# Optimization experiments

Hardware: AMD Instinct MI355X
Metric: run time of the kernel (lower is better)

## Reference

```python
import jax, jax.numpy as jnp
import numpy as np
from jax import lax

INPUT_SCALE = 1.0
RES_SCALE = 1.0


def setup_inputs() -> dict:
    key = jax.random.key(0)
    k1, k2, k3, k4 = jax.random.split(key, 4)
    seq_len, input_size, res_size = 4096, 512, 2048
    return {
        "input_data": jax.random.normal(k1, (seq_len, input_size), dtype=jnp.float32),
        "initial_state": jax.random.normal(k2, (res_size,), dtype=jnp.float32),
        "W_in": jax.random.normal(k3, (res_size, input_size), dtype=jnp.float32),
        "W_res": jax.random.normal(k4, (res_size, res_size), dtype=jnp.float32),
    }


def reference(input_data, initial_state, W_in, W_res):
    # state_t = tanh(input_scale * W_in @ x_t + res_scale * W_res @ state_{t-1}) / sqrt(res_size)
    res_size = W_res.shape[0]
    inv_sqrt = jnp.asarray(1.0 / np.sqrt(res_size), dtype=input_data.dtype)
    # Precompute input projection for all timesteps as one GEMM: (seq_len, res_size)
    pre = (INPUT_SCALE * input_data) @ W_in.T

    def step(state, u_t):
        new_state = jnp.tanh(u_t + RES_SCALE * (W_res @ state)) * inv_sqrt
        return new_state, new_state

    _, states = lax.scan(step, initial_state, pre)
    # (seq_len + 1, res_size): row 0 is the initial state
    return jnp.concatenate([initial_state[None, :], states], axis=0)
```

## Files before the change

### kernel.cpp

```cpp
#include <hip/hip_runtime.h>

constexpr int SEQ  = 4096;
constexpr int IN   = 512;
constexpr int RS   = 2048;
constexpr int GB   = 64;
constexpr int BT   = 1024;
constexpr int RING = 8;
constexpr float INV_SQRT = 0.022097086912079612f;

__global__ __launch_bounds__(256)
void gemm_pre_kernel(const float* __restrict__ A, const float* __restrict__ B,
                     float* __restrict__ out) {
    __shared__ float As[64][17];
    __shared__ float Bs[64][17];
    const int tid = threadIdx.x;
    const int tx = tid & 15, ty = tid >> 4;
    const int m0 = blockIdx.x * 64, n0 = blockIdx.y * 64;
    const int lr = tid >> 2;
    const int lk = (tid & 3) * 4;
    float acc[4][4] = {};
    for (int k0 = 0; k0 < IN; k0 += 16) {
        const float4 av = *(const float4*)&A[(size_t)(m0 + lr) * IN + k0 + lk];
        const float4 bv = *(const float4*)&B[(size_t)(n0 + lr) * IN + k0 + lk];
        __syncthreads();
        As[lr][lk + 0] = av.x; As[lr][lk + 1] = av.y;
        As[lr][lk + 2] = av.z; As[lr][lk + 3] = av.w;
        Bs[lr][lk + 0] = bv.x; Bs[lr][lk + 1] = bv.y;
        Bs[lr][lk + 2] = bv.z; Bs[lr][lk + 3] = bv.w;
        __syncthreads();
#pragma unroll
        for (int k = 0; k < 16; ++k) {
            float a[4], b[4];
#pragma unroll
            for (int i = 0; i < 4; ++i) a[i] = As[ty * 4 + i][k];
#pragma unroll
            for (int j = 0; j < 4; ++j) b[j] = Bs[tx * 4 + j][k];
#pragma unroll
            for (int i = 0; i < 4; ++i)
#pragma unroll
                for (int j = 0; j < 4; ++j) acc[i][j] += a[i] * b[j];
        }
    }
#pragma unroll
    for (int i = 0; i < 4; ++i) {
        float4 v = make_float4(acc[i][0], acc[i][1], acc[i][2], acc[i][3]);
        *(float4*)&out[(size_t)(m0 + ty * 4 + i + 1) * RS + n0 + tx * 4] = v;
    }
}

__device__ __forceinline__ float fast_tanh(float x) {
    float e = __expf(2.0f * x);
    return 1.0f - 2.0f * __builtin_amdgcn_rcpf(e + 1.0f);
}

#define AT_LOAD_U64(p) __hip_atomic_load((p), __ATOMIC_RELAXED, __HIP_MEMORY_SCOPE_AGENT)
#define AT_STORE_U32(p, v) __hip_atomic_store((p), (v), __ATOMIC_RELAXED, __HIP_MEMORY_SCOPE_AGENT)

__global__ __launch_bounds__(BT, 4)
void reservoir_scan_kernel(const float* __restrict__ W_res,
                           const float* __restrict__ init,
                           float* __restrict__ out,
                           unsigned* __restrict__ ring) {
    __shared__ float s_state[RS];
    __shared__ float s_pub[32];
    const int bid  = blockIdx.x;
    const int tid  = threadIdx.x;
    const int wave = tid >> 6;
    const int lane = tid & 63;
    const int r0   = bid * 32 + wave * 2;

    const float* wp0 = W_res + (size_t)r0 * RS + lane * 4;
    const float* wp1 = wp0 + RS;
    float4 w0[8], w1[8];
#pragma unroll
    for (int j = 0; j < 8; ++j) {
        w0[j] = *(const float4*)(wp0 + j * 256);
        w1[j] = *(const float4*)(wp1 + j * 256);
    }
#pragma unroll
    for (int j = 0; j < 8; ++j) {
        asm volatile("" : "+v"(w0[j].x), "+v"(w0[j].y), "+v"(w0[j].z), "+v"(w0[j].w));
        asm volatile("" : "+v"(w1[j].x), "+v"(w1[j].y), "+v"(w1[j].z), "+v"(w1[j].w));
    }

    if (wave == 0 && lane < 32) {
        float v = init[bid * 32 + lane];
        out[bid * 32 + lane] = v;
        AT_STORE_U32(ring + bid * 32 + lane, __float_as_uint(v + 1.0f));
    }

    for (int t = 0; t < SEQ; ++t) {
        const size_t crow = (size_t)(t & (RING - 1)) * RS;
        const size_t prow = (size_t)((t + 1) & (RING - 1)) * RS;
        const size_t zrow = (size_t)((t + 2) & (RING - 1)) * RS;

        float pre = 0.f;
        if (lane < 2) pre = out[(size_t)(t + 1) * RS + r0 + lane];

        {
            const unsigned long long* pp =
                reinterpret_cast<const unsigned long long*>(ring + crow) + tid;
            unsigned long long v = AT_LOAD_U64(pp);
            while (((unsigned)v == 0u) || ((unsigned)(v >> 32) == 0u))
                v = AT_LOAD_U64(pp);
            s_state[2 * tid]     = __uint_as_float((unsigned)v) - 1.0f;
            s_state[2 * tid + 1] = __uint_as_float((unsigned)(v >> 32)) - 1.0f;
        }
        __syncthreads();

        if (wave == 0 && lane < 32)
            AT_STORE_U32(ring + zrow + bid * 32 + lane, 0u);

        float a0 = 0.f, a1 = 0.f;
#pragma unroll
        for (int j = 0; j < 8; ++j) {
            const float4 sv = *(const float4*)&s_state[lane * 4 + j * 256];
            a0 += w0[j].x * sv.x + w0[j].y * sv.y + w0[j].z * sv.z + w0[j].w * sv.w;
            a1 += w1[j].x * sv.x + w1[j].y * sv.y + w1[j].z * sv.z + w1[j].w * sv.w;
        }
#pragma unroll
        for (int off = 32; off > 0; off >>= 1) {
            a0 += __shfl_xor(a0, off);
            a1 += __shfl_xor(a1, off);
        }

        if (lane < 2) {
            float a = lane ? a1 : a0;
            float s = fast_tanh(pre + a) * INV_SQRT;
            out[(size_t)(t + 1) * RS + r0 + lane] = s;
            s_pub[wave * 2 + lane] = s + 1.0f;
        }
        __syncthreads();

        if (wave == 0 && lane < 32) {
            asm volatile("s_waitcnt vmcnt(0)" ::: "memory");
            AT_STORE_U32(ring + prow + bid * 32 + lane,
                         __float_as_uint(s_pub[lane]));
        }
    }
}

extern "C" void kernel_launch(void* const* d_in, const int* in_sizes, int n_in,
                              void* d_out, int out_size, void* d_ws, size_t ws_size,
                              hipStream_t stream) {
    const float* x     = (const float*)d_in[0];
    const float* init  = (const float*)d_in[1];
    const float* W_in  = (const float*)d_in[2];
    const float* W_res = (const float*)d_in[3];
    float* out = (float*)d_out;
    unsigned* ring = (unsigned*)d_ws;

    hipMemsetAsync(d_ws, 0, (size_t)RING * RS * sizeof(float), stream);
    gemm_pre_kernel<<<dim3(SEQ / 64, RS / 64), 256, 0, stream>>>(x, W_in, out);

    void* args[] = { (void*)&W_res, (void*)&init, (void*)&out, (void*)&ring };
    hipLaunchCooperativeKernel((void*)reservoir_scan_kernel,
                               dim3(GB), dim3(BT), args, 0, stream);
}
```

Measured before the change: 8.383 ms.

## Publish state per wave with packed 64-bit stores and double-buffered shared state

After: 19.37 ms. +131.1%, slower.

```diff
diff --git a/kernel.cpp b/kernel.cpp
--- a/kernel.cpp
+++ b/kernel.cpp
@@ -53,21 +53,27 @@
     return 1.0f - 2.0f * __builtin_amdgcn_rcpf(e + 1.0f);
 }
 
-#define AT_LOAD_U64(p) __hip_atomic_load((p), __ATOMIC_RELAXED, __HIP_MEMORY_SCOPE_AGENT)
-#define AT_STORE_U32(p, v) __hip_atomic_store((p), (v), __ATOMIC_RELAXED, __HIP_MEMORY_SCOPE_AGENT)
+typedef unsigned long long u64;
+#define AT_LOAD_U64(p)     __hip_atomic_load((p), __ATOMIC_RELAXED, __HIP_MEMORY_SCOPE_AGENT)
+#define AT_STORE_U64(p, v) __hip_atomic_store((p), (v), __ATOMIC_RELAXED, __HIP_MEMORY_SCOPE_AGENT)
+
+__device__ __forceinline__ u64 enc2(float a, float b) {
+    return (u64)(__float_as_uint(a) | 1u) |
+           ((u64)(__float_as_uint(b) | 1u) << 32);
+}
 
 __global__ __launch_bounds__(BT, 4)
 void reservoir_scan_kernel(const float* __restrict__ W_res,
                            const float* __restrict__ init,
                            float* __restrict__ out,
-                           unsigned* __restrict__ ring) {
-    __shared__ float s_state[RS];
-    __shared__ float s_pub[32];
+                           u64* __restrict__ ring) {
+    __shared__ float s_state[2][RS];
     const int bid  = blockIdx.x;
     const int tid  = threadIdx.x;
     const int wave = tid >> 6;
     const int lane = tid & 63;
     const int r0   = bid * 32 + wave * 2;
+    const int slot = r0 >> 1;
 
     const float* wp0 = W_res + (size_t)r0 * RS + lane * 4;
     const float* wp1 = wp0 + RS;
@@ -83,38 +89,39 @@
         asm volatile("" : "+v"(w1[j].x), "+v"(w1[j].y), "+v"(w1[j].z), "+v"(w1[j].w));
     }
 
-    if (wave == 0 && lane < 32) {
-        float v = init[bid * 32 + lane];
-        out[bid * 32 + lane] = v;
-        AT_STORE_U32(ring + bid * 32 + lane, __float_as_uint(v + 1.0f));
+    if (lane == 0) {
+        float2 v = *(const float2*)(init + r0);
+        *(float2*)(out + r0) = v;
+        asm volatile("s_waitcnt vmcnt(0)" ::: "memory");
+        AT_STORE_U64(ring + slot, enc2(v.x, v.y));
     }
 
     for (int t = 0; t < SEQ; ++t) {
-        const size_t crow = (size_t)(t & (RING - 1)) * RS;
-        const size_t prow = (size_t)((t + 1) & (RING - 1)) * RS;
-        const size_t zrow = (size_t)((t + 2) & (RING - 1)) * RS;
+        const size_t crow = (size_t)(t & (RING - 1)) * (RS / 2);
+        const size_t prow = (size_t)((t + 1) & (RING - 1)) * (RS / 2);
+        const size_t zrow = (size_t)((t + 2) & (RING - 1)) * (RS / 2);
 
-        float pre = 0.f;
-        if (lane < 2) pre = out[(size_t)(t + 1) * RS + r0 + lane];
+        float2 pf;
+        if (lane == 0) {
+            AT_STORE_U64(ring + zrow + slot, 0ull);
+            pf = *(const float2*)(out + (size_t)(t + 1) * RS + r0);
+        }
 
+        float* sb = s_state[t & 1];
         {
-            const unsigned long long* pp =
-                reinterpret_cast<const unsigned long long*>(ring + crow) + tid;
-            unsigned long long v = AT_LOAD_U64(pp);
+            const u64* pp = ring + crow + tid;
+            u64 v = AT_LOAD_U64(pp);
             while (((unsigned)v == 0u) || ((unsigned)(v >> 32) == 0u))
                 v = AT_LOAD_U64(pp);
-            s_state[2 * tid]     = __uint_as_float((unsigned)v) - 1.0f;
-            s_state[2 * tid + 1] = __uint_as_float((unsigned)(v >> 32)) - 1.0f;
+            sb[2 * tid]     = __uint_as_float((unsigned)v);
+            sb[2 * tid + 1] = __uint_as_float((unsigned)(v >> 32));
         }
         __syncthreads();
-
-        if (wave == 0 && lane < 32)
-            AT_STORE_U32(ring + zrow + bid * 32 + lane, 0u);
 
         float a0 = 0.f, a1 = 0.f;
 #pragma unroll
         for (int j = 0; j < 8; ++j) {
-            const float4 sv = *(const float4*)&s_state[lane * 4 + j * 256];
+            const float4 sv = *(const float4*)&sb[lane * 4 + j * 256];
             a0 += w0[j].x * sv.x + w0[j].y * sv.y + w0[j].z * sv.z + w0[j].w * sv.w;
             a1 += w1[j].x * sv.x + w1[j].y * sv.y + w1[j].z * sv.z + w1[j].w * sv.w;
         }
@@ -124,18 +131,12 @@
             a1 += __shfl_xor(a1, off);
         }
 
-        if (lane < 2) {
-            float a = lane ? a1 : a0;
-            float s = fast_tanh(pre + a) * INV_SQRT;
-            out[(size_t)(t + 1) * RS + r0 + lane] = s;
-            s_pub[wave * 2 + lane] = s + 1.0f;
-        }
-        __syncthreads();
-
-        if (wave == 0 && lane < 32) {
+        if (lane == 0) {
+            float s0 = fast_tanh(pf.x + a0) * INV_SQRT;
+            float s1 = fast_tanh(pf.y + a1) * INV_SQRT;
+            *(float2*)(out + (size_t)(t + 1) * RS + r0) = make_float2(s0, s1);
             asm volatile("s_waitcnt vmcnt(0)" ::: "memory");
-            AT_STORE_U32(ring + prow + bid * 32 + lane,
-                         __float_as_uint(s_pub[lane]));
+            AT_STORE_U64(ring + prow + slot, enc2(s0, s1));
         }
     }
 }
@@ -148,7 +149,7 @@
     const float* W_in  = (const float*)d_in[2];
     const float* W_res = (const float*)d_in[3];
     float* out = (float*)d_out;
-    unsigned* ring = (unsigned*)d_ws;
+    u64* ring = (u64*)d_ws;
 
     hipMemsetAsync(d_ws, 0, (size_t)RING * RS * sizeof(float), stream);
     gemm_pre_kernel<<<dim3(SEQ / 64, RS / 64), 256, 0, stream>>>(x, W_in, out);
```
